# Kernel optimization log

Measured on AMD Instinct MI355X. Metric: run time of the kernel, lower is better.

Reference implementation:

```python
import jax, jax.numpy as jnp
import numpy as np

N_FFT = 800
HOP = 200
WIN = 800
FREQ = N_FFT // 2 + 1  # 401
B, T = 32, 480000


def _make_weights():
    # periodic hann window
    n = np.arange(N_FFT)
    window = 0.5 - 0.5 * np.cos(2.0 * np.pi * np.arange(WIN) / WIN)
    k = np.arange(FREQ)
    angle = 2.0 * np.pi * np.outer(k, n) / N_FFT  # [FREQ, N_FFT]
    fwd_real = (np.cos(angle) * window).astype(np.float32)
    fwd_imag = (-np.sin(angle) * window).astype(np.float32)
    angle_t = 2.0 * np.pi * np.outer(n, k) / N_FFT  # [N_FFT, FREQ]
    inv_window = window * (1.0 / N_FFT)
    bwd_real = (np.cos(angle_t).T * inv_window).astype(np.float32)  # [FREQ, N_FFT]
    bwd_imag = (np.sin(angle_t).T * inv_window).astype(np.float32)
    return (jnp.asarray(fwd_real), jnp.asarray(fwd_imag),
            jnp.asarray(bwd_real), jnp.asarray(bwd_imag))


def setup_inputs() -> dict:
    key = jax.random.key(0)
    x = jax.random.normal(key, (B, T), dtype=jnp.float32)
    wfr, wfi, wbr, wbi = _make_weights()
    return {"x": x, "w_fwd_real": wfr, "w_fwd_imag": wfi,
            "w_bwd_real": wbr, "w_bwd_imag": wbi}


def reference(x, w_fwd_real, w_fwd_imag, w_bwd_real, w_bwd_imag):
    Tlen = x.shape[-1]
    pad = N_FFT // 2
    xp = jnp.pad(x, ((0, 0), (pad, pad)), mode="edge")  # replicate pad
    n_frames = (xp.shape[-1] - N_FFT) // HOP + 1
    # frame extraction (== conv1d stride HOP with dense DFT kernels)
    fidx = jnp.arange(n_frames)[:, None] * HOP + jnp.arange(N_FFT)[None, :]
    frames = xp[:, fidx]  # [B, F, N_FFT]
    real = jnp.einsum("bfn,kn->bkf", frames, w_fwd_real)  # [B, FREQ, F]
    imag = jnp.einsum("bfn,kn->bkf", frames, w_fwd_imag)
    magnitude = jnp.sqrt(real * real + imag * imag + 1e-14)
    phase = jnp.arctan2(imag, real)
    phase = jnp.where((imag == 0) & (real < 0), jnp.pi, phase)
    # inverse: iDFT-as-GEMM + overlap-add (== conv_transpose1d stride HOP)
    rp = magnitude * jnp.cos(phase)
    ip = magnitude * jnp.sin(phase)
    yr = jnp.einsum("bkf,kn->bfn", rp, w_bwd_real)  # [B, F, N_FFT]
    yi = jnp.einsum("bkf,kn->bfn", ip, w_bwd_imag)
    y_frames = yr - yi
    l_out = (n_frames - 1) * HOP + N_FFT
    oidx = jnp.arange(n_frames)[:, None] * HOP + jnp.arange(N_FFT)[None, :]
    wave = jnp.zeros((x.shape[0], l_out), dtype=x.dtype).at[:, oidx].add(y_frames)
    return wave[:, pad:pad + Tlen]
```

## Files before the change

kernel.cpp:

```cpp
#include <hip/hip_runtime.h>
#include <math.h>

#define HOP     200
#define NB      32
#define TLEN    480000
#define TLEN4   (TLEN / 4)
#define SEG     20
#define NTILE   (TLEN / HOP / SEG)
#define NSEGP   (SEG + 6)
#define NW4     (50 * NSEGP)
#define DOFF    150

#define DLT  0.00785398163397448f
#define C1K  0.99996915760f
#define S1K  0.00785390090f
#define C2K  0.99987663248f
#define S2K  0.01570731731f
#define C3K  0.99972243010f
#define S3K  0.02355976470f
#define C40  0.95105651629515f
#define S40  0.30901699437495f

typedef float floatx4 __attribute__((ext_vector_type(4)));

__global__ __launch_bounds__(256) void stft_tile(const float* __restrict__ x,
                                                 float* __restrict__ out) {
    __shared__ float4 xw4[NW4];
    __shared__ float  part[NSEGP][10][6];
    __shared__ float  pg[NSEGP][6];
    __shared__ float4 segc[2][SEG];

    const int qb = blockIdx.x;
    const int b  = blockIdx.y;
    const int q0 = qb * SEG;
    const float* xb = x + (size_t)b * TLEN;
    const float4* xg = (const float4*)xb;

    {
        const int jg0 = 50 * (q0 - 3);
        float4 r[6];
#pragma unroll
        for (int i = 0; i < 6; ++i) {
            const int j = threadIdx.x + 256 * i;
            if (j < NW4) {
                const int jg = jg0 + j;
                if (jg < 0) {
                    const float e = xb[0];
                    r[i] = make_float4(e, e, e, e);
                } else if (jg >= TLEN4) {
                    const float e = xb[TLEN - 1];
                    r[i] = make_float4(e, e, e, e);
                } else {
                    r[i] = xg[jg];
                }
            }
        }
#pragma unroll
        for (int i = 0; i < 6; ++i) {
            const int j = threadIdx.x + 256 * i;
            if (j < NW4) xw4[j] = r[i];
        }
    }
    __syncthreads();

    for (int u = threadIdx.x; u < NSEGP * 10; u += 256) {
        const int s = u / 10;
        const int k = u - 10 * s;
        const int g = q0 - 3 + s;
        const int gm = (g + 4) & 3;
        float c0, sn0;
        __sincosf((float)(gm * 200 + 4 * k) * DLT, &sn0, &c0);

        float4 v[5];
#pragma unroll
        for (int i = 0; i < 5; ++i) v[i] = xw4[50 * s + k + 10 * i];

        float p1e = 0.f, p1o = 0.f, pce = 0.f, pco = 0.f, pse = 0.f, pso = 0.f;
#pragma unroll
        for (int i = 0; i < 5; ++i) {
            const float c1 = c0 * C1K - sn0 * S1K, s1 = sn0 * C1K + c0 * S1K;
            const float c2 = c0 * C2K - sn0 * S2K, s2 = sn0 * C2K + c0 * S2K;
            const float c3 = c0 * C3K - sn0 * S3K, s3 = sn0 * C3K + c0 * S3K;
            p1e += v[i].x + v[i].z;             p1o += v[i].y + v[i].w;
            pce += c0 * v[i].x + c2 * v[i].z;   pco += c1 * v[i].y + c3 * v[i].w;
            pse += sn0 * v[i].x + s2 * v[i].z;  pso += s1 * v[i].y + s3 * v[i].w;
            const float cn = c0 * C40 - sn0 * S40;
            sn0 = sn0 * C40 + c0 * S40;  c0 = cn;
        }
        part[s][k][0] = p1e;  part[s][k][1] = p1o;
        part[s][k][2] = pce;  part[s][k][3] = pco;
        part[s][k][4] = pse;  part[s][k][5] = pso;
    }
    __syncthreads();

    for (int u = threadIdx.x; u < NSEGP * 6; u += 256) {
        const int s = u / 6;
        const int c = u - 6 * s;
        float a = 0.f;
#pragma unroll
        for (int k = 0; k < 10; ++k) a += part[s][k][c];
        pg[s][c] = a;
    }
    __syncthreads();

    if (threadIdx.x < 2 * SEG) {
        const int par = threadIdx.x & 1;
        const int ql  = threadIdx.x >> 1;
        const int q   = q0 + ql;
        float A = 0.f, C = 0.f, D = 0.f;
#pragma unroll
        for (int df = -1; df <= 2; ++df) {
            const int f = q + df;
            if (f < 0 || f > 2400) continue;
            const int ls0 = f - q0 + 1;
            float sp1 = 0.f, spc = 0.f, sps = 0.f;
#pragma unroll
            for (int kk = 0; kk < 4; ++kk) {
                const float* rec = pg[ls0 + kk];
                sp1 += rec[par];  spc += rec[2 + par];  sps += rec[4 + par];
            }
            const int fm = f & 3;
            const float tr = (fm == 0) ? spc : (fm == 1) ? sps : (fm == 2) ? -spc : -sps;
            const float S = 0.5f * sp1 + 0.5f * tr;
            A += S;
            if (fm == 0) C += S; else if (fm == 2) C -= S;
            else if (fm == 1) D += S; else D -= S;
        }
        segc[par][ql] = make_float4(A * (1.0f / 1600.0f),
                                    sqrtf(C * C + D * D) * (1.0f / 1600.0f),
                                    atan2f(D, C), 0.f);
    }
    __syncthreads();

    const bool headblk = (qb == 0);
    const bool tailblk = (qb == NTILE - 1);
    floatx4* og4 = (floatx4*)(out + (size_t)b * TLEN + HOP * q0);
    const int pmb = (q0 & 3) * 200 + 400;
    for (int j = threadIdx.x; j < 50 * SEG; j += 256) {
        const float4 xv = xw4[DOFF + j];
        const int sl = j / 50;
        const float4 ce = segc[0][sl];
        const float4 co = segc[1][sl];
        const int pm = (pmb + 4 * j) % 800;
        const float xa[4] = {xv.x, xv.y, xv.z, xv.w};
        float r[4];
#pragma unroll
        for (int c = 0; c < 4; ++c) {
            const float4 cc = (c & 1) ? co : ce;
            r[c] = 0.75f * xa[c] + cc.x - cc.y * __cosf((float)(pm + c) * DLT - cc.z);
        }
        if (headblk && sl == 0) {
#pragma unroll
            for (int c = 0; c < 4; ++c) {
                const float wm = 0.5f + 0.5f * __sinf((float)(pm + c) * DLT);
                r[c] -= 0.5f * wm * wm * xa[c];
            }
        }
        if (tailblk && sl == SEG - 1) {
#pragma unroll
            for (int c = 0; c < 4; ++c) {
                const float wm = 0.5f - 0.5f * __sinf((float)(pm + c) * DLT);
                r[c] -= 0.5f * wm * wm * xa[c];
            }
        }
        floatx4 rv = {r[0], r[1], r[2], r[3]};
        __builtin_nontemporal_store(rv, &og4[j]);
    }
}

extern "C" void kernel_launch(void* const* d_in, const int* in_sizes, int n_in,
                              void* d_out, int out_size, void* d_ws, size_t ws_size,
                              hipStream_t stream) {
    const float* x = (const float*)d_in[0];
    float* out = (float*)d_out;
    stft_tile<<<dim3(NTILE, NB), dim3(256), 0, stream>>>(x, out);
}
```

Measured before the change: 120.7 us.

## Process three tiles per block with register prefetch of next tile input

Each block now handles three consecutive tiles instead of one, and cuts the grid in x by three. While computing the current tile, it issues the global loads for the next tile into registers, then writes them to shared memory after the output phase. Block barriers are replaced by an inline-asm LDS-wait plus s_barrier, which skips waiting on outstanding global loads. The aim is to hide global load latency and amortise launch cost per block. In exchange, registers stay live across phases and there are fewer blocks to spread across CUs.

```diff
diff --git a/kernel.cpp b/kernel.cpp
--- a/kernel.cpp
+++ b/kernel.cpp
@@ -7,6 +7,8 @@
 #define TLEN4   (TLEN / 4)
 #define SEG     20
 #define NTILE   (TLEN / HOP / SEG)
+#define NTPB    3
+#define NBLKX   (NTILE / NTPB)
 #define NSEGP   (SEG + 6)
 #define NW4     (50 * NSEGP)
 #define DOFF    150
@@ -23,6 +25,8 @@
 
 typedef float floatx4 __attribute__((ext_vector_type(4)));
 
+#define LBAR() asm volatile("s_waitcnt lgkmcnt(0)\n\ts_barrier" ::: "memory")
+
 __global__ __launch_bounds__(256) void stft_tile(const float* __restrict__ x,
                                                  float* __restrict__ out) {
     __shared__ float4 xw4[NW4];
@@ -30,18 +34,18 @@
     __shared__ float  pg[NSEGP][6];
     __shared__ float4 segc[2][SEG];
 
-    const int qb = blockIdx.x;
     const int b  = blockIdx.y;
-    const int q0 = qb * SEG;
+    const int t0 = blockIdx.x * NTPB;
     const float* xb = x + (size_t)b * TLEN;
     const float4* xg = (const float4*)xb;
 
-    {
-        const int jg0 = 50 * (q0 - 3);
-        float4 r[6];
+    float4 r[6];
+
+    auto stage_load = [&](int t) {
+        const int jg0 = 1000 * t - 150;
 #pragma unroll
         for (int i = 0; i < 6; ++i) {
-            const int j = threadIdx.x + 256 * i;
+            const int j = (int)threadIdx.x + 256 * i;
             if (j < NW4) {
                 const int jg = jg0 + j;
                 if (jg < 0) {
@@ -55,116 +59,135 @@
                 }
             }
         }
+    };
+    auto stage_write = [&]() {
 #pragma unroll
         for (int i = 0; i < 6; ++i) {
-            const int j = threadIdx.x + 256 * i;
+            const int j = (int)threadIdx.x + 256 * i;
             if (j < NW4) xw4[j] = r[i];
         }
-    }
-    __syncthreads();
-
-    for (int u = threadIdx.x; u < NSEGP * 10; u += 256) {
-        const int s = u / 10;
-        const int k = u - 10 * s;
-        const int g = q0 - 3 + s;
-        const int gm = (g + 4) & 3;
-        float c0, sn0;
-        __sincosf((float)(gm * 200 + 4 * k) * DLT, &sn0, &c0);
-
-        float4 v[5];
-#pragma unroll
-        for (int i = 0; i < 5; ++i) v[i] = xw4[50 * s + k + 10 * i];
-
-        float p1e = 0.f, p1o = 0.f, pce = 0.f, pco = 0.f, pse = 0.f, pso = 0.f;
-#pragma unroll
-        for (int i = 0; i < 5; ++i) {
-            const float c1 = c0 * C1K - sn0 * S1K, s1 = sn0 * C1K + c0 * S1K;
-            const float c2 = c0 * C2K - sn0 * S2K, s2 = sn0 * C2K + c0 * S2K;
-            const float c3 = c0 * C3K - sn0 * S3K, s3 = sn0 * C3K + c0 * S3K;
-            p1e += v[i].x + v[i].z;             p1o += v[i].y + v[i].w;
-            pce += c0 * v[i].x + c2 * v[i].z;   pco += c1 * v[i].y + c3 * v[i].w;
-            pse += sn0 * v[i].x + s2 * v[i].z;  pso += s1 * v[i].y + s3 * v[i].w;
-            const float cn = c0 * C40 - sn0 * S40;
-            sn0 = sn0 * C40 + c0 * S40;  c0 = cn;
-        }
-        part[s][k][0] = p1e;  part[s][k][1] = p1o;
-        part[s][k][2] = pce;  part[s][k][3] = pco;
-        part[s][k][4] = pse;  part[s][k][5] = pso;
-    }
-    __syncthreads();
-
-    for (int u = threadIdx.x; u < NSEGP * 6; u += 256) {
-        const int s = u / 6;
-        const int c = u - 6 * s;
-        float a = 0.f;
-#pragma unroll
-        for (int k = 0; k < 10; ++k) a += part[s][k][c];
-        pg[s][c] = a;
-    }
-    __syncthreads();
-
-    if (threadIdx.x < 2 * SEG) {
-        const int par = threadIdx.x & 1;
-        const int ql  = threadIdx.x >> 1;
-        const int q   = q0 + ql;
-        float A = 0.f, C = 0.f, D = 0.f;
-#pragma unroll
-        for (int df = -1; df <= 2; ++df) {
-            const int f = q + df;
-            if (f < 0 || f > 2400) continue;
-            const int ls0 = f - q0 + 1;
-            float sp1 = 0.f, spc = 0.f, sps = 0.f;
-#pragma unroll
-            for (int kk = 0; kk < 4; ++kk) {
-                const float* rec = pg[ls0 + kk];
-                sp1 += rec[par];  spc += rec[2 + par];  sps += rec[4 + par];
-            }
-            const int fm = f & 3;
-            const float tr = (fm == 0) ? spc : (fm == 1) ? sps : (fm == 2) ? -spc : -sps;
-            const float S = 0.5f * sp1 + 0.5f * tr;
-            A += S;
-            if (fm == 0) C += S; else if (fm == 2) C -= S;
-            else if (fm == 1) D += S; else D -= S;
-        }
-        segc[par][ql] = make_float4(A * (1.0f / 1600.0f),
-                                    sqrtf(C * C + D * D) * (1.0f / 1600.0f),
-                                    atan2f(D, C), 0.f);
-    }
-    __syncthreads();
-
-    const bool headblk = (qb == 0);
-    const bool tailblk = (qb == NTILE - 1);
-    floatx4* og4 = (floatx4*)(out + (size_t)b * TLEN + HOP * q0);
-    const int pmb = (q0 & 3) * 200 + 400;
-    for (int j = threadIdx.x; j < 50 * SEG; j += 256) {
-        const float4 xv = xw4[DOFF + j];
-        const int sl = j / 50;
-        const float4 ce = segc[0][sl];
-        const float4 co = segc[1][sl];
-        const int pm = (pmb + 4 * j) % 800;
-        const float xa[4] = {xv.x, xv.y, xv.z, xv.w};
-        float r[4];
-#pragma unroll
-        for (int c = 0; c < 4; ++c) {
-            const float4 cc = (c & 1) ? co : ce;
-            r[c] = 0.75f * xa[c] + cc.x - cc.y * __cosf((float)(pm + c) * DLT - cc.z);
-        }
-        if (headblk && sl == 0) {
+    };
+
+    stage_load(t0);
+    stage_write();
+    LBAR();
+
+    for (int tt = 0; tt < NTPB; ++tt) {
+        const int t  = t0 + tt;
+        const int q0 = t * SEG;
+        const bool pf = (tt + 1 < NTPB);
+
+        if (pf) stage_load(t + 1);
+
+        for (int u = threadIdx.x; u < NSEGP * 10; u += 256) {
+            const int s = u / 10;
+            const int k = u - 10 * s;
+            const int g = q0 - 3 + s;
+            const int gm = (g + 4) & 3;
+            float c0, sn0;
+            __sincosf((float)(gm * 200 + 4 * k) * DLT, &sn0, &c0);
+
+            float4 v[5];
+#pragma unroll
+            for (int i = 0; i < 5; ++i) v[i] = xw4[50 * s + k + 10 * i];
+
+            float p1e = 0.f, p1o = 0.f, pce = 0.f, pco = 0.f, pse = 0.f, pso = 0.f;
+#pragma unroll
+            for (int i = 0; i < 5; ++i) {
+                const float c1 = c0 * C1K - sn0 * S1K, s1 = sn0 * C1K + c0 * S1K;
+                const float c2 = c0 * C2K - sn0 * S2K, s2 = sn0 * C2K + c0 * S2K;
+                const float c3 = c0 * C3K - sn0 * S3K, s3 = sn0 * C3K + c0 * S3K;
+                p1e += v[i].x + v[i].z;             p1o += v[i].y + v[i].w;
+                pce += c0 * v[i].x + c2 * v[i].z;   pco += c1 * v[i].y + c3 * v[i].w;
+                pse += sn0 * v[i].x + s2 * v[i].z;  pso += s1 * v[i].y + s3 * v[i].w;
+                const float cn = c0 * C40 - sn0 * S40;
+                sn0 = sn0 * C40 + c0 * S40;  c0 = cn;
+            }
+            part[s][k][0] = p1e;  part[s][k][1] = p1o;
+            part[s][k][2] = pce;  part[s][k][3] = pco;
+            part[s][k][4] = pse;  part[s][k][5] = pso;
+        }
+        LBAR();
+
+        for (int u = threadIdx.x; u < NSEGP * 6; u += 256) {
+            const int s = u / 6;
+            const int c = u - 6 * s;
+            float a = 0.f;
+#pragma unroll
+            for (int k = 0; k < 10; ++k) a += part[s][k][c];
+            pg[s][c] = a;
+        }
+        LBAR();
+
+        if (threadIdx.x < 2 * SEG) {
+            const int par = threadIdx.x & 1;
+            const int ql  = threadIdx.x >> 1;
+            const int q   = q0 + ql;
+            float A = 0.f, C = 0.f, D = 0.f;
+#pragma unroll
+            for (int df = -1; df <= 2; ++df) {
+                const int f = q + df;
+                if (f < 0 || f > 2400) continue;
+                const int ls0 = f - q0 + 1;
+                float sp1 = 0.f, spc = 0.f, sps = 0.f;
+#pragma unroll
+                for (int kk = 0; kk < 4; ++kk) {
+                    const float* rec = pg[ls0 + kk];
+                    sp1 += rec[par];  spc += rec[2 + par];  sps += rec[4 + par];
+                }
+                const int fm = f & 3;
+                const float tr = (fm == 0) ? spc : (fm == 1) ? sps : (fm == 2) ? -spc : -sps;
+                const float S = 0.5f * sp1 + 0.5f * tr;
+                A += S;
+                if (fm == 0) C += S; else if (fm == 2) C -= S;
+                else if (fm == 1) D += S; else D -= S;
+            }
+            segc[par][ql] = make_float4(A * (1.0f / 1600.0f),
+                                        sqrtf(C * C + D * D) * (1.0f / 1600.0f),
+                                        atan2f(D, C), 0.f);
+        }
+        LBAR();
+
+        const bool headblk = (t == 0);
+        const bool tailblk = (t == NTILE - 1);
+        floatx4* og4 = (floatx4*)(out + (size_t)b * TLEN + HOP * q0);
+        const int pmb = (q0 & 3) * 200 + 400;
+        for (int j = threadIdx.x; j < 50 * SEG; j += 256) {
+            const float4 xv = xw4[DOFF + j];
+            const int sl = j / 50;
+            const float4 ce = segc[0][sl];
+            const float4 co = segc[1][sl];
+            const int pm = (pmb + 4 * j) % 800;
+            const float xa[4] = {xv.x, xv.y, xv.z, xv.w};
+            float rr[4];
 #pragma unroll
             for (int c = 0; c < 4; ++c) {
-                const float wm = 0.5f + 0.5f * __sinf((float)(pm + c) * DLT);
-                r[c] -= 0.5f * wm * wm * xa[c];
-            }
-        }
-        if (tailblk && sl == SEG - 1) {
-#pragma unroll
-            for (int c = 0; c < 4; ++c) {
-                const float wm = 0.5f - 0.5f * __sinf((float)(pm + c) * DLT);
-                r[c] -= 0.5f * wm * wm * xa[c];
-            }
-        }
-        floatx4 rv = {r[0], r[1], r[2], r[3]};
-        __builtin_nontemporal_store(rv, &og4[j]);
+                const float4 cc = (c & 1) ? co : ce;
+                rr[c] = 0.75f * xa[c] + cc.x - cc.y * __cosf((float)(pm + c) * DLT - cc.z);
+            }
+            if (headblk && sl == 0) {
+#pragma unroll
+                for (int c = 0; c < 4; ++c) {
+                    const float wm = 0.5f + 0.5f * __sinf((float)(pm + c) * DLT);
+                    rr[c] -= 0.5f * wm * wm * xa[c];
+                }
+            }
+            if (tailblk && sl == SEG - 1) {
+#pragma unroll
+                for (int c = 0; c < 4; ++c) {
+                    const float wm = 0.5f - 0.5f * __sinf((float)(pm + c) * DLT);
+                    rr[c] -= 0.5f * wm * wm * xa[c];
+                }
+            }
+            floatx4 rv = {rr[0], rr[1], rr[2], rr[3]};
+            __builtin_nontemporal_store(rv, &og4[j]);
+        }
+
+        if (pf) {
+            LBAR();
+            stage_write();
+            LBAR();
+        }
     }
 }
 
@@ -173,5 +196,5 @@
                               hipStream_t stream) {
     const float* x = (const float*)d_in[0];
     float* out = (float*)d_out;
-    stft_tile<<<dim3(NTILE, NB), dim3(256), 0, stream>>>(x, out);
+    stft_tile<<<dim3(NBLKX, NB), dim3(256), 0, stream>>>(x, out);
 }
```

New measurement: 141.2 us. 1.17x slower.
